# Kernel tuning notes

Measured on AMD Instinct MI355X. Metric: run time of the kernel, lower is better.

## Reference

```python
import jax, jax.numpy as jnp
import numpy as np

V, D, H, L, F, S, HI, DI, TOPK = 50257, 1024, 16, 8, 4096, 1024, 4, 64, 512
DH = D // H
EPS = 1e-6


def rmsnorm(x, w):
    # matches torch: norm = ||x||_2 * D^-0.5 ; out = w * x / (norm + eps)
    n = jnp.linalg.norm(x, axis=-1, keepdims=True) * (x.shape[-1] ** -0.5)
    return w * (x / (n + EPS))


def setup_inputs() -> dict:
    key = jax.random.key(0)
    ks = jax.random.split(key, 16)
    std = 0.02
    tokens = jax.random.randint(ks[0], (2, S), 0, V)
    embed_w = jax.random.normal(ks[1], (V, D), jnp.float32) * std
    pos_w = jax.random.normal(ks[2], (S, D), jnp.float32) * std
    wq = jax.random.normal(ks[3], (L, D, D), jnp.float32) * std
    wk = jax.random.normal(ks[4], (L, D, D), jnp.float32) * std
    wv = jax.random.normal(ks[5], (L, D, D), jnp.float32) * std
    wo = jax.random.normal(ks[6], (L, D, D), jnp.float32) * std
    iq = jax.random.normal(ks[7], (L, D, HI * DI), jnp.float32) * std
    ik = jax.random.normal(ks[8], (L, D, DI), jnp.float32) * std
    iw = jax.random.normal(ks[9], (L, D, HI), jnp.float32) * std
    w1 = jax.random.normal(ks[10], (L, D, F), jnp.float32) * std
    w2 = jax.random.normal(ks[11], (L, F, D), jnp.float32) * std
    norm1 = jnp.ones((L, D), jnp.float32)
    norm2 = jnp.ones((L, D), jnp.float32)
    norm_f = jnp.ones((D,), jnp.float32)
    return dict(tokens=tokens, embed_w=embed_w, pos_w=pos_w, wq=wq, wk=wk,
                wv=wv, wo=wo, iq=iq, ik=ik, iw=iw, w1=w1, w2=w2,
                norm1=norm1, norm2=norm2, norm_f=norm_f)


def _block(x, p, causal):
    (wq, wk, wv, wo, iq, ik, iw, w1, w2, n1, n2) = p
    B = x.shape[0]
    NEG = jnp.finfo(x.dtype).min
    h = rmsnorm(x, n1)
    # --- lightning indexer: scores [B, S, S] ---
    qi = (h @ iq).reshape(B, S, HI, DI)          # [B,S,HI,DI]
    ki = h @ ik                                   # [B,S,DI]
    wt = h @ iw                                   # [B,S,HI]
    idx_logits = jax.nn.relu(jnp.einsum('bqhd,bkd->bhqk', qi, ki))
    idx_scores = jnp.einsum('bqh,bhqk->bqk', wt, idx_logits)  # [B,S,S]
    masked_idx = jnp.where(causal, idx_scores, NEG)
    _, top_i = jax.lax.top_k(masked_idx, TOPK)    # [B,S,TOPK]
    bi = jnp.arange(B)[:, None, None]
    qix = jnp.arange(S)[None, :, None]
    topk_mask = jnp.zeros((B, S, S), bool).at[bi, qix, top_i].set(True)
    allowed = causal & topk_mask                  # [B,S,S]
    # --- sparse multi-head attention (masked dense form, same math) ---
    q = (h @ wq).reshape(B, S, H, DH)
    k = (h @ wk).reshape(B, S, H, DH)
    v = (h @ wv).reshape(B, S, H, DH)
    att = jnp.einsum('bqhd,bkhd->bhqk', q, k) / jnp.sqrt(jnp.float32(DH))
    att = jnp.where(allowed[:, None, :, :], att, NEG)
    p_att = jax.nn.softmax(att, axis=-1)
    out = jnp.einsum('bhqk,bkhd->bqhd', p_att, v).reshape(B, S, D) @ wo
    x = x + out
    # --- feed-forward (exact GELU as nn.GELU) ---
    h2 = rmsnorm(x, n2)
    x = x + jax.nn.gelu(h2 @ w1, approximate=False) @ w2
    return x


def reference(tokens, embed_w, pos_w, wq, wk, wv, wo, iq, ik, iw, w1, w2,
              norm1, norm2, norm_f):
    x = embed_w[tokens] + pos_w[None, :tokens.shape[1], :]
    causal = jnp.tril(jnp.ones((S, S), bool))[None]  # [1,S,S]

    def step(x, p):
        return _block(x, p, causal), None

    x, _ = jax.lax.scan(step, x, (wq, wk, wv, wo, iq, ik, iw, w1, w2, norm1, norm2))
    x = rmsnorm(x, norm_f)
    logits = x @ embed_w.T  # tied lm_head
    return logits
```

## Files before the change

kernel.cpp:

```cpp
#include <hip/hip_runtime.h>
#include <cstdint>
#include <cstddef>

#define S_LEN 1024
#define D_DIM 1024
#define NH 16
#define DHD 64
#define NL 8
#define FF_DIM 4096
#define HI_N 4
#define DI_N 64
#define TOPK_N 512
#define BSROWS 2048
#define VOCAB 50257
#define VPAD 50304
#define NTILES_V 393
#define YPX 50

#define QKV_LD 3072
#define IDX_LD 384
#define COL_QI 0
#define COL_KI 256
#define COL_WT 320

#define NEGF -3.0e38f

typedef __attribute__((ext_vector_type(8))) _Float16 half8;
typedef __attribute__((ext_vector_type(4))) _Float16 half4v;
typedef __attribute__((ext_vector_type(4))) float f32x4;

#if __has_builtin(__builtin_amdgcn_mfma_f32_16x16x16f16)
#define MFMA16F(a, b, c) __builtin_amdgcn_mfma_f32_16x16x16f16((a), (b), (c), 0, 0, 0)
#else
static __device__ __forceinline__ f32x4 mfma16f_asm(half4v a, half4v b, f32x4 c) {
  f32x4 d;
  asm volatile("v_mfma_f32_16x16x16_f16 %0, %1, %2, %3\n\ts_nop 7\n\ts_nop 7"
               : "=v"(d) : "v"(a), "v"(b), "v"(c));
  return d;
}
#define MFMA16F(a, b, c) mfma16f_asm((a), (b), (c))
#endif

typedef const __attribute__((address_space(1))) void* gas_ptr;
typedef __attribute__((address_space(3))) void* las_ptr;
__device__ __forceinline__ void gload16(const void* g, void* l) {
#if __has_builtin(__builtin_amdgcn_global_load_lds)
  __builtin_amdgcn_global_load_lds((gas_ptr)g, (las_ptr)l, 16, 0, 0);
#else
  *(uint4*)l = *(const uint4*)g;
#endif
}

__device__ __forceinline__ short f2h(float x) {
  _Float16 h = (_Float16)x;
  return *reinterpret_cast<short*>(&h);
}
__device__ __forceinline__ float h2f(short b) {
  _Float16 h = *reinterpret_cast<_Float16*>(&b);
  return (float)h;
}
__device__ __forceinline__ void split_h(float x, short& hi, short& lo) {
  hi = f2h(x);
  lo = f2h(x - h2f(hi));
}

__global__ __launch_bounds__(256) void embed_kernel(
    const int* __restrict__ tokens, const float* __restrict__ E,
    const float* __restrict__ P, float* __restrict__ X)
{
  int bs = blockIdx.x;
  int s = bs & (S_LEN - 1);
  int tid = threadIdx.x;
  int tok = tokens[bs];
  float4 e = ((const float4*)(E + (size_t)tok * D_DIM))[tid];
  float4 p = ((const float4*)(P + (size_t)s * D_DIM))[tid];
  float4 o; o.x = e.x + p.x; o.y = e.y + p.y; o.z = e.z + p.z; o.w = e.w + p.w;
  ((float4*)(X + (size_t)bs * D_DIM))[tid] = o;
}

__global__ __launch_bounds__(256) void cvt_embed_kernel(
    const float* __restrict__ E, short* __restrict__ Eh)
{
  const long valid4 = (long)VOCAB * D_DIM / 4;
  const long total4 = (long)VPAD * D_DIM / 4;
  long i = (long)blockIdx.x * 256 + threadIdx.x;
  long stride = (long)gridDim.x * 256;
  for (; i < total4; i += stride) {
    short4 o = make_short4(0, 0, 0, 0);
    if (i < valid4) {
      float4 v = ((const float4*)E)[i];
      o = make_short4(f2h(v.x), f2h(v.y), f2h(v.z), f2h(v.w));
    }
    ((short4*)Eh)[i] = o;
  }
}

__global__ __launch_bounds__(256) void rmsnorm_split_kernel(
    const float* __restrict__ X, const float* __restrict__ W,
    short* __restrict__ O )
{
  int r = blockIdx.x;
  int tid = threadIdx.x;
  float4 v = ((const float4*)(X + (size_t)r * D_DIM))[tid];
  float ss = v.x * v.x + v.y * v.y + v.z * v.z + v.w * v.w;
  __shared__ float red[4];
  __shared__ float sh_inv;
  for (int o = 32; o; o >>= 1) ss += __shfl_down(ss, o);
  if ((tid & 63) == 0) red[tid >> 6] = ss;
  __syncthreads();
  if (tid == 0) {
    float s = red[0] + red[1] + red[2] + red[3];
    sh_inv = 1.0f / (sqrtf(s) * 0.03125f + 1e-6f);
  }
  __syncthreads();
  float inv = sh_inv;
  float4 w = ((const float4*)W)[tid];
  float o0 = w.x * v.x * inv, o1 = w.y * v.y * inv;
  float o2 = w.z * v.z * inv, o3 = w.w * v.w * inv;
  short4 hi, lo;
  split_h(o0, hi.x, lo.x); split_h(o1, hi.y, lo.y);
  split_h(o2, hi.z, lo.z); split_h(o3, hi.w, lo.w);
  ((short4*)(O + (size_t)r * D_DIM))[tid] = hi;
  ((short4*)(O + (size_t)BSROWS * D_DIM + (size_t)r * D_DIM))[tid] = lo;
}

__global__ __launch_bounds__(256) void rmsnorm_h_kernel(
    const float* __restrict__ X, const float* __restrict__ W, short* __restrict__ O)
{
  int r = blockIdx.x;
  int tid = threadIdx.x;
  float4 v = ((const float4*)(X + (size_t)r * D_DIM))[tid];
  float ss = v.x * v.x + v.y * v.y + v.z * v.z + v.w * v.w;
  __shared__ float red[4];
  __shared__ float sh_inv;
  for (int o = 32; o; o >>= 1) ss += __shfl_down(ss, o);
  if ((tid & 63) == 0) red[tid >> 6] = ss;
  __syncthreads();
  if (tid == 0) {
    float s = red[0] + red[1] + red[2] + red[3];
    sh_inv = 1.0f / (sqrtf(s) * 0.03125f + 1e-6f);
  }
  __syncthreads();
  float inv = sh_inv;
  float4 w = ((const float4*)W)[tid];
  short4 o4 = make_short4(f2h(w.x * v.x * inv), f2h(w.y * v.y * inv),
                          f2h(w.z * v.z * inv), f2h(w.w * v.w * inv));
  ((short4*)(O + (size_t)r * D_DIM))[tid] = o4;
}

__global__ __launch_bounds__(256) void packT_all_kernel(
    const float* __restrict__ W0, short* __restrict__ BT0, int K, int N)
{
  __shared__ float t[32][33];
  int z = blockIdx.z;
  const float* W = W0 + (size_t)z * K * N;
  short* BT = BT0 + (size_t)z * N * K;
  int n0 = blockIdx.x * 32, k0 = blockIdx.y * 32;
  int tx = threadIdx.x, ty = threadIdx.y;
#pragma unroll
  for (int r = 0; r < 32; r += 8)
    t[ty + r][tx] = W[(size_t)(k0 + ty + r) * N + n0 + tx];
  __syncthreads();
#pragma unroll
  for (int r = 0; r < 32; r += 8)
    BT[(size_t)(n0 + ty + r) * K + k0 + tx] = f2h(t[tx][ty + r]);
}

__global__ __launch_bounds__(256) void pack_qkv_all_kernel(
    const float* __restrict__ wq0, const float* __restrict__ wk0,
    const float* __restrict__ wv0, short* __restrict__ BT0)
{
  __shared__ float t[32][33];
  int z = blockIdx.z;
  const float* wq = wq0 + (size_t)z * D_DIM * D_DIM;
  const float* wk = wk0 + (size_t)z * D_DIM * D_DIM;
  const float* wv = wv0 + (size_t)z * D_DIM * D_DIM;
  short* BT = BT0 + (size_t)z * QKV_LD * D_DIM;
  int n0 = blockIdx.x * 32, k0 = blockIdx.y * 32;
  int tx = threadIdx.x, ty = threadIdx.y;
  const float* src = (n0 < 1024) ? wq : (n0 < 2048) ? wk : wv;
  int c0 = n0 & 1023;
#pragma unroll
  for (int r = 0; r < 32; r += 8)
    t[ty + r][tx] = src[(size_t)(k0 + ty + r) * 1024 + c0 + tx];
  __syncthreads();
#pragma unroll
  for (int r = 0; r < 32; r += 8)
    BT[(size_t)(n0 + ty + r) * D_DIM + k0 + tx] = f2h(t[tx][ty + r]);
}

__global__ __launch_bounds__(256) void pack_idx_all_kernel(
    const float* __restrict__ iq0, const float* __restrict__ ik0,
    const float* __restrict__ iw0, short* __restrict__ BT0)
{
  __shared__ float t[32][33];
  const size_t plane = (size_t)IDX_LD * D_DIM;
  int z = blockIdx.z;
  const float* iq = iq0 + (size_t)z * D_DIM * (HI_N * DI_N);
  const float* ik = ik0 + (size_t)z * D_DIM * DI_N;
  const float* iw = iw0 + (size_t)z * D_DIM * HI_N;
  short* BT = BT0 + (size_t)z * 2 * plane;
  int n0 = blockIdx.x * 32, k0 = blockIdx.y * 32;
  int tx = threadIdx.x, ty = threadIdx.y;
  const float* src = nullptr; int ld = 0, c0 = 0;
  if (n0 < 256)      { src = iq; ld = 256; c0 = n0; }
  else if (n0 < 320) { src = ik; ld = 64;  c0 = n0 - 256; }
  else if (n0 < 352) { src = iw; ld = 4;   c0 = n0 - 320; }
#pragma unroll
  for (int r = 0; r < 32; r += 8) {
    float v = 0.f;
    int c = c0 + tx;
    if (src && c < ld) v = src[(size_t)(k0 + ty + r) * ld + c];
    t[ty + r][tx] = v;
  }
  __syncthreads();
#pragma unroll
  for (int r = 0; r < 32; r += 8) {
    short hi, lo;
    split_h(t[tx][ty + r], hi, lo);
    size_t o = (size_t)(n0 + ty + r) * D_DIM + k0 + tx;
    BT[o] = hi;
    BT[plane + o] = lo;
  }
}

#define RA 40

template<int BM>
__global__ __launch_bounds__(256) void gemm_split_kernel(
    const short* __restrict__ A, size_t aplane,
    const short* __restrict__ BT, size_t bplane,
    float* __restrict__ C, int M, int N, int K)
{
  constexpr int MI = BM / 32;
  __shared__ short Al[2 * BM * RA];
  __shared__ short Bl[2 * 128 * RA];
  int tid = threadIdx.x;
  int wave = tid >> 6, lane = tid & 63;
  int wr = (wave >> 1) * (BM / 2), wc = (wave & 1) * 64;
  int lr = lane & 15, lk = lane >> 4;
  int m0 = blockIdx.y * BM, n0 = blockIdx.x * 128;
  f32x4 acc[MI][4] = {};

  for (int k0 = 0; k0 < K; k0 += 32) {
    __syncthreads();
#pragma unroll
    for (int f = 0; f < BM / 32; ++f) {
      int idx = tid + f * 256;
      int p = idx / (BM * 4), r2 = idx % (BM * 4);
      int row = r2 >> 2, sub = r2 & 3;
      uint4 v = *(const uint4*)(A + (size_t)p * aplane + (size_t)(m0 + row) * K + k0 + sub * 8);
      *(uint4*)(Al + p * BM * RA + row * RA + sub * 8) = v;
    }
#pragma unroll
    for (int f = 0; f < 4; ++f) {
      int idx = tid + f * 256;
      int p = idx >> 9, r2 = idx & 511;
      int row = r2 >> 2, sub = r2 & 3;
      uint4 v = *(const uint4*)(BT + (size_t)p * bplane + (size_t)(n0 + row) * K + k0 + sub * 8);
      *(uint4*)(Bl + p * 128 * RA + row * RA + sub * 8) = v;
    }
    __syncthreads();
    half8 ah[MI], al_[MI], bh[4], bl_[4];
#pragma unroll
    for (int i = 0; i < MI; ++i) {
      ah[i] = *(const half8*)(Al + (wr + i * 16 + lr) * RA + lk * 8);
      al_[i] = *(const half8*)(Al + BM * RA + (wr + i * 16 + lr) * RA + lk * 8);
    }
#pragma unroll
    for (int j = 0; j < 4; ++j) {
      bh[j] = *(const half8*)(Bl + (wc + j * 16 + lr) * RA + lk * 8);
      bl_[j] = *(const half8*)(Bl + 128 * RA + (wc + j * 16 + lr) * RA + lk * 8);
    }
#pragma unroll
    for (int i = 0; i < MI; ++i)
#pragma unroll
      for (int j = 0; j < 4; ++j) {
        f32x4 a = acc[i][j];
        a = __builtin_amdgcn_mfma_f32_16x16x32_f16(al_[i], bh[j], a, 0, 0, 0);
        a = __builtin_amdgcn_mfma_f32_16x16x32_f16(ah[i], bl_[j], a, 0, 0, 0);
        a = __builtin_amdgcn_mfma_f32_16x16x32_f16(ah[i], bh[j], a, 0, 0, 0);
        acc[i][j] = a;
      }
  }
#pragma unroll
  for (int i = 0; i < MI; ++i)
#pragma unroll
    for (int r = 0; r < 4; ++r) {
      int m = m0 + wr + i * 16 + lk * 4 + r;
#pragma unroll
      for (int j = 0; j < 4; ++j) {
        int n = n0 + wc + j * 16 + lr;
        if (n < N) C[(size_t)m * N + n] = acc[i][j][r];
      }
    }
}

template<int BM, int EPI>
__global__ __launch_bounds__(256) void gemm_g_kernel(
    const short* __restrict__ A, const short* __restrict__ BT,
    const float* __restrict__ R, void* __restrict__ C, int M, int N, int K)
{
  constexpr int MI = BM / 32;
  constexpr int AF = (BM >= 64) ? BM / 64 : 1;
  __shared__ short Al[BM * 32];
  __shared__ short Bl[128 * 32];
  int tid = threadIdx.x;
  int wave = tid >> 6, lane = tid & 63;
  int wr = (wave >> 1) * (BM / 2), wc = (wave & 1) * 64;
  int lr = lane & 15, lk = lane >> 4;
  int m0 = blockIdx.y * BM, n0 = blockIdx.x * 128;
  f32x4 acc[MI][4] = {};

  const short* ap[AF]; short* ad[AF];
#pragma unroll
  for (int f = 0; f < AF; ++f) {
    int idx = tid + f * 256;
    int row = idx >> 2, slot = idx & 3;
    ap[f] = A + (size_t)(m0 + row) * K + ((slot ^ (row & 3)) * 8);
    ad[f] = Al + idx * 8;
  }
  const bool a_act = (BM >= 64) || (tid < BM * 4);
  const short* bp[2]; short* bd[2];
#pragma unroll
  for (int f = 0; f < 2; ++f) {
    int idx = tid + f * 256;
    int row = idx >> 2, slot = idx & 3;
    bp[f] = BT + (size_t)(n0 + row) * K + ((slot ^ (row & 3)) * 8);
    bd[f] = Bl + idx * 8;
  }
  int aoff[MI], boff[4];
#pragma unroll
  for (int i = 0; i < MI; ++i) {
    int row = wr + i * 16 + lr;
    aoff[i] = row * 32 + ((lk ^ (row & 3)) * 8);
  }
#pragma unroll
  for (int j = 0; j < 4; ++j) {
    int row = wc + j * 16 + lr;
    boff[j] = row * 32 + ((lk ^ (row & 3)) * 8);
  }

  for (int k0 = 0; k0 < K; k0 += 32) {
    __syncthreads();
#pragma unroll
    for (int f = 0; f < AF; ++f)
      if (a_act) { gload16(ap[f], ad[f]); ap[f] += 32; }
#pragma unroll
    for (int f = 0; f < 2; ++f) { gload16(bp[f], bd[f]); bp[f] += 32; }
    __syncthreads();
    half8 af[MI], bfr[4];
#pragma unroll
    for (int i = 0; i < MI; ++i) af[i] = *(const half8*)(Al + aoff[i]);
#pragma unroll
    for (int j = 0; j < 4; ++j) bfr[j] = *(const half8*)(Bl + boff[j]);
#pragma unroll
    for (int i = 0; i < MI; ++i)
#pragma unroll
      for (int j = 0; j < 4; ++j)
        acc[i][j] = __builtin_amdgcn_mfma_f32_16x16x32_f16(af[i], bfr[j], acc[i][j], 0, 0, 0);
  }
#pragma unroll
  for (int i = 0; i < MI; ++i)
#pragma unroll
    for (int r = 0; r < 4; ++r) {
      int m = m0 + wr + i * 16 + lk * 4 + r;
#pragma unroll
      for (int j = 0; j < 4; ++j) {
        int n = n0 + wc + j * 16 + lr;
        float v = acc[i][j][r];
        if (EPI == 1) {
          ((short*)C)[(size_t)m * N + n] = f2h(v);
        } else if (EPI == 2) {
          v = 0.5f * v * (1.0f + erff(v * 0.70710678118654752f));
          ((short*)C)[(size_t)m * N + n] = f2h(v);
        } else {
          ((float*)C)[(size_t)m * N + n] = v + R[(size_t)m * N + n];
        }
      }
    }
}

__global__ __launch_bounds__(256) void gemm_logits_g_kernel(
    const short* __restrict__ A, const short* __restrict__ BT,
    float* __restrict__ C, int M, int N, int K)
{
  int bid = blockIdx.x;
  int xcd = bid & 7, idx0 = bid >> 3;
  int mt = idx0 & 15, yt = (idx0 >> 4) + xcd * YPX;
  if (yt >= NTILES_V) return;
  int m0 = mt * 128, n0 = yt * 128;

  __shared__ short Al[128 * 32];
  __shared__ short Bl[128 * 32];
  int tid = threadIdx.x;
  int wave = tid >> 6, lane = tid & 63;
  int wr = (wave >> 1) * 64, wc = (wave & 1) * 64;
  int lr = lane & 15, lk = lane >> 4;
  f32x4 acc[4][4] = {};

  const short* ap[2]; short* ad[2];
  const short* bp[2]; short* bd[2];
#pragma unroll
  for (int f = 0; f < 2; ++f) {
    int idx = tid + f * 256;
    int row = idx >> 2, slot = idx & 3;
    ap[f] = A + (size_t)(m0 + row) * K + ((slot ^ (row & 3)) * 8);
    ad[f] = Al + idx * 8;
    bp[f] = BT + (size_t)(n0 + row) * K + ((slot ^ (row & 3)) * 8);
    bd[f] = Bl + idx * 8;
  }
  int aoff[4], boff[4];
#pragma unroll
  for (int i = 0; i < 4; ++i) {
    int row = wr + i * 16 + lr;
    aoff[i] = row * 32 + ((lk ^ (row & 3)) * 8);
    int rowb = wc + i * 16 + lr;
    boff[i] = rowb * 32 + ((lk ^ (rowb & 3)) * 8);
  }

  for (int k0 = 0; k0 < K; k0 += 32) {
    __syncthreads();
#pragma unroll
    for (int f = 0; f < 2; ++f) { gload16(ap[f], ad[f]); ap[f] += 32; }
#pragma unroll
    for (int f = 0; f < 2; ++f) { gload16(bp[f], bd[f]); bp[f] += 32; }
    __syncthreads();
    half8 af[4], bfr[4];
#pragma unroll
    for (int i = 0; i < 4; ++i) af[i] = *(const half8*)(Al + aoff[i]);
#pragma unroll
    for (int j = 0; j < 4; ++j) bfr[j] = *(const half8*)(Bl + boff[j]);
#pragma unroll
    for (int i = 0; i < 4; ++i)
#pragma unroll
      for (int j = 0; j < 4; ++j)
        acc[i][j] = __builtin_amdgcn_mfma_f32_16x16x32_f16(af[i], bfr[j], acc[i][j], 0, 0, 0);
  }
#pragma unroll
  for (int i = 0; i < 4; ++i)
#pragma unroll
    for (int r = 0; r < 4; ++r) {
      int m = m0 + wr + i * 16 + lk * 4 + r;
#pragma unroll
      for (int j = 0; j < 4; ++j) {
        int n = n0 + wc + j * 16 + lr;
        if (n < N) C[(size_t)m * N + n] = acc[i][j][r];
      }
    }
}

__global__ __launch_bounds__(256) void gemm_logits_f32b_kernel(
    const short* __restrict__ A, const float* __restrict__ BT,
    float* __restrict__ C, int M, int N, int K)
{
  __shared__ short Al[128 * RA];
  __shared__ short Bl[128 * RA];
  int tid = threadIdx.x;
  int wave = tid >> 6, lane = tid & 63;
  int wr = (wave >> 1) * 64, wc = (wave & 1) * 64;
  int lr = lane & 15, lk = lane >> 4;
  int m0 = blockIdx.y * 128, n0 = blockIdx.x * 128;
  f32x4 acc[4][4] = {};

  for (int k0 = 0; k0 < K; k0 += 32) {
    __syncthreads();
#pragma unroll
    for (int f = 0; f < 2; ++f) {
      int idx = tid + f * 256, row = idx >> 2, sub = idx & 3;
      uint4 v = *(const uint4*)(A + (size_t)(m0 + row) * K + k0 + sub * 8);
      *(uint4*)(Al + row * RA + sub * 8) = v;
    }
#pragma unroll
    for (int f = 0; f < 4; ++f) {
      int idx = tid + f * 256, row = idx >> 3, qq = idx & 7;
      int gn = n0 + row;
      float4 v = make_float4(0.f, 0.f, 0.f, 0.f);
      if (gn < N) v = *(const float4*)(BT + (size_t)gn * K + k0 + qq * 4);
      *(short4*)(Bl + row * RA + qq * 4) =
          make_short4(f2h(v.x), f2h(v.y), f2h(v.z), f2h(v.w));
    }
    __syncthreads();
    half8 af[4], bfr[4];
#pragma unroll
    for (int i = 0; i < 4; ++i)
      af[i] = *(const half8*)(Al + (wr + i * 16 + lr) * RA + lk * 8);
#pragma unroll
    for (int j = 0; j < 4; ++j)
      bfr[j] = *(const half8*)(Bl + (wc + j * 16 + lr) * RA + lk * 8);
#pragma unroll
    for (int i = 0; i < 4; ++i)
#pragma unroll
      for (int j = 0; j < 4; ++j)
        acc[i][j] = __builtin_amdgcn_mfma_f32_16x16x32_f16(af[i], bfr[j], acc[i][j], 0, 0, 0);
  }
#pragma unroll
  for (int i = 0; i < 4; ++i)
#pragma unroll
    for (int r = 0; r < 4; ++r) {
      int m = m0 + wr + i * 16 + lk * 4 + r;
#pragma unroll
      for (int j = 0; j < 4; ++j) {
        int n = n0 + wc + j * 16 + lr;
        if (n < N) C[(size_t)m * N + n] = acc[i][j][r];
      }
    }
}

__device__ __forceinline__ unsigned int ford(float f) {
  unsigned int u = __float_as_uint(f);
  return (u & 0x80000000u) ? ~u : (u | 0x80000000u);
}

__global__ __launch_bounds__(256) void idx_topk_kernel(
    const float* __restrict__ Hx, unsigned int* __restrict__ MASK)
{
  int bq = blockIdx.x;
  int q = bq & (S_LEN - 1);
  int b = bq >> 10;
  int tid = threadIdx.x;
  int n = q + 1;
  if (n <= TOPK_N) {
    if (tid < 32) {
      int full = n >> 5, rem = n & 31;
      unsigned int w = 0u;
      if (tid < full) w = 0xFFFFFFFFu;
      else if (tid == full && rem) w = (1u << rem) - 1u;
      MASK[(size_t)bq * 32 + tid] = w;
    }
    return;
  }
  __shared__ float qi_s[HI_N * DI_N];
  __shared__ float wt_s[HI_N];
  __shared__ float sc[S_LEN];
  __shared__ unsigned long long keys[S_LEN];
  __shared__ unsigned int mw[32];
  qi_s[tid] = Hx[(size_t)bq * IDX_LD + COL_QI + tid];
  if (tid < HI_N) wt_s[tid] = Hx[(size_t)bq * IDX_LD + COL_WT + tid];
  __syncthreads();
  for (int k = tid; k < n; k += 256) {
    const float* kr = Hx + (size_t)(b * S_LEN + k) * IDX_LD + COL_KI;
    float d0 = 0.f, d1 = 0.f, d2 = 0.f, d3 = 0.f;
#pragma unroll
    for (int d = 0; d < DI_N; ++d) {
      float kv = kr[d];
      d0 = fmaf(qi_s[d], kv, d0);
      d1 = fmaf(qi_s[64 + d], kv, d1);
      d2 = fmaf(qi_s[128 + d], kv, d2);
      d3 = fmaf(qi_s[192 + d], kv, d3);
    }
    sc[k] = wt_s[0] * fmaxf(d0, 0.f) + wt_s[1] * fmaxf(d1, 0.f)
          + wt_s[2] * fmaxf(d2, 0.f) + wt_s[3] * fmaxf(d3, 0.f);
  }
  __syncthreads();
  for (int i = tid; i < S_LEN; i += 256) {
    unsigned long long kk = 0ull;
    if (i < n) kk = ((unsigned long long)ford(sc[i]) << 32) | (unsigned int)(S_LEN - 1 - i);
    keys[i] = kk;
  }
  __syncthreads();
  for (int size = 2; size <= S_LEN; size <<= 1) {
    for (int stride = size >> 1; stride > 0; stride >>= 1) {
      for (int t = tid; t < S_LEN / 2; t += 256) {
        int j = t & (stride - 1);
        int lo = ((t ^ j) << 1) | j;
        int hi = lo | stride;
        unsigned long long a = keys[lo], c = keys[hi];
        bool desc = ((lo & size) == 0);
        bool sw = desc ? (a < c) : (a > c);
        if (sw) { keys[lo] = c; keys[hi] = a; }
      }
      __syncthreads();
    }
  }
  if (tid < 32) mw[tid] = 0u;
  __syncthreads();
  for (int i = tid; i < TOPK_N; i += 256) {
    int k = S_LEN - 1 - (int)(keys[i] & 0xFFFFFFFFull);
    atomicOr(&mw[k >> 5], 1u << (k & 31));
  }
  __syncthreads();
  if (tid < 32) MASK[(size_t)bq * 32 + tid] = mw[tid];
}

__global__ __launch_bounds__(256) void attn_mfma_kernel(
    const short* __restrict__ QKV, const unsigned int* __restrict__ MASK,
    short* __restrict__ O )
{
  __shared__ unsigned int mlds[64 * 32];
  __shared__ short Kl[2][64 * 64];
  __shared__ short Vtl[2][64 * 68];
  int i = blockIdx.x;
  int p = i >> 5;
  int qt = (p < 8) ? p : 23 - p;
  int h = (i >> 1) & 15;
  int b = i & 1;
  int tid = threadIdx.x;
  int w = tid >> 6, l = tid & 63;
  int lq = l & 15, g = l >> 4;
  int q0 = qt * 64;
  const short* Kb = QKV + (size_t)b * S_LEN * QKV_LD + 1024 + h * DHD;
  const short* Vb = QKV + (size_t)b * S_LEN * QKV_LD + 2048 + h * DHD;
  int vu = tid >> 1, vhalf = tid & 1, vkg = vu >> 3, vdg = vu & 7;

#pragma unroll
  for (int i2 = 0; i2 < 8; ++i2) {
    int idx = tid + i2 * 256;
    mlds[idx] = MASK[((size_t)(b * S_LEN + q0 + (idx >> 5))) * 32 + (idx & 31)];
  }
  half8 qf[2];
  {
    const short* qrow = QKV + ((size_t)(b * S_LEN + q0 + w * 16 + lq)) * QKV_LD + h * DHD;
    qf[0] = *(const half8*)(qrow + g * 8);
    qf[1] = *(const half8*)(qrow + 32 + g * 8);
  }
  {
#pragma unroll
    for (int i2 = 0; i2 < 2; ++i2) {
      int idx = tid + i2 * 256;
      int row = idx >> 3, sub = idx & 7;
      gload16(Kb + (size_t)row * QKV_LD + (size_t)((sub ^ (row & 7)) * 8), &Kl[0][idx * 8]);
    }
    int krow = vkg * 4 + vhalf * 2;
    uint4 v0 = *(const uint4*)(Vb + (size_t)krow * QKV_LD + vdg * 8);
    uint4 v1 = *(const uint4*)(Vb + (size_t)(krow + 1) * QKV_LD + vdg * 8);
    const short* s0 = (const short*)&v0;
    const short* s1 = (const short*)&v1;
#pragma unroll
    for (int j = 0; j < 8; ++j)
      *(short2*)(&Vtl[0][(vdg * 8 + j) * 68 + vkg * 4 + vhalf * 2]) = make_short2(s0[j], s1[j]);
  }
  __syncthreads();

  f32x4 acc_o[4] = {};
  float m_run = -1.0e30f, l_run = 0.f;
  const int mrow = w * 16 + lq;
  int cur = 0;

  for (int kt = 0; kt <= qt; ++kt) {
    bool more = kt < qt;
    uint4 v0, v1;
    if (more) {
#pragma unroll
      for (int i2 = 0; i2 < 2; ++i2) {
        int idx = tid + i2 * 256;
        int row = idx >> 3, sub = idx & 7;
        gload16(Kb + (size_t)((kt + 1) * 64 + row) * QKV_LD + (size_t)((sub ^ (row & 7)) * 8),
                &Kl[cur ^ 1][idx * 8]);
      }
      int krow = (kt + 1) * 64 + vkg * 4 + vhalf * 2;
      v0 = *(const uint4*)(Vb + (size_t)krow * QKV_LD + vdg * 8);
      v1 = *(const uint4*)(Vb + (size_t)(krow + 1) * QKV_LD + vdg * 8);
    }
    f32x4 s[4] = {};
    __builtin_amdgcn_s_setprio(1);
#pragma unroll
    for (int ks = 0; ks < 4; ++ks) {
      half8 kf0 = *(const half8*)(&Kl[cur][(ks * 16 + lq) * 64 + ((g ^ (lq & 7)) * 8)]);
      half8 kf1 = *(const half8*)(&Kl[cur][(ks * 16 + lq) * 64 + (((4 + g) ^ (lq & 7)) * 8)]);
      s[ks] = __builtin_amdgcn_mfma_f32_16x16x32_f16(kf0, qf[0], s[ks], 0, 0, 0);
      s[ks] = __builtin_amdgcn_mfma_f32_16x16x32_f16(kf1, qf[1], s[ks], 0, 0, 0);
    }
    __builtin_amdgcn_s_setprio(0);
    float mx = NEGF;
#pragma unroll
    for (int ks = 0; ks < 4; ++ks) {
      int kbase = kt * 64 + ks * 16 + g * 4;
      unsigned mwv = mlds[mrow * 32 + (kbase >> 5)];
#pragma unroll
      for (int r = 0; r < 4; ++r) {
        float sv = ((mwv >> ((kbase + r) & 31)) & 1u) ? s[ks][r] * 0.125f : NEGF;
        s[ks][r] = sv;
        mx = fmaxf(mx, sv);
      }
    }
    mx = fmaxf(mx, __shfl_xor(mx, 16));
    mx = fmaxf(mx, __shfl_xor(mx, 32));
    float m_new = fmaxf(m_run, mx);
    float scale = __expf(m_run - m_new);
    float lsum = 0.f;
    half4v pf[4];
#pragma unroll
    for (int ks = 0; ks < 4; ++ks) {
      half4v t;
#pragma unroll
      for (int r = 0; r < 4; ++r) {
        float pp = __expf(s[ks][r] - m_new);
        lsum += pp;
        t[r] = (_Float16)pp;
      }
      pf[ks] = t;
    }
    lsum += __shfl_xor(lsum, 16);
    lsum += __shfl_xor(lsum, 32);
    l_run = l_run * scale + lsum;
    m_run = m_new;
    float sc[4];
#pragma unroll
    for (int r = 0; r < 4; ++r) sc[r] = __shfl(scale, g * 4 + r);
    __builtin_amdgcn_s_setprio(1);
#pragma unroll
    for (int dt = 0; dt < 4; ++dt) {
      f32x4 a = acc_o[dt];
      a[0] *= sc[0]; a[1] *= sc[1]; a[2] *= sc[2]; a[3] *= sc[3];
#pragma unroll
      for (int ks = 0; ks < 4; ++ks) {
        half4v vf = *(const half4v*)(&Vtl[cur][(dt * 16 + lq) * 68 + ks * 16 + g * 4]);
        a = MFMA16F(pf[ks], vf, a);
      }
      acc_o[dt] = a;
    }
    __builtin_amdgcn_s_setprio(0);
    if (more) {
      const short* s0 = (const short*)&v0;
      const short* s1 = (const short*)&v1;
#pragma unroll
      for (int j = 0; j < 8; ++j)
        *(short2*)(&Vtl[cur ^ 1][(vdg * 8 + j) * 68 + vkg * 4 + vhalf * 2]) = make_short2(s0[j], s1[j]);
    }
    __syncthreads();
    cur ^= 1;
  }
  float linv[4];
#pragma unroll
  for (int r = 0; r < 4; ++r) linv[r] = 1.0f / __shfl(l_run, g * 4 + r);
#pragma unroll
  for (int dt = 0; dt < 4; ++dt)
#pragma unroll
    for (int r = 0; r < 4; ++r) {
      int q = q0 + w * 16 + g * 4 + r;
      float o = acc_o[dt][r] * linv[r];
      O[(size_t)(b * S_LEN + q) * D_DIM + h * DHD + dt * 16 + lq] = f2h(o);
    }
}

extern "C" void kernel_launch(void* const* d_in, const int* in_sizes, int n_in,
                              void* d_out, int out_size, void* d_ws, size_t ws_size,
                              hipStream_t stream) {
  (void)in_sizes; (void)n_in; (void)out_size;
  const int*   tokens  = (const int*)d_in[0];
  const float* embed_w = (const float*)d_in[1];
  const float* pos_w   = (const float*)d_in[2];
  const float* wq      = (const float*)d_in[3];
  const float* wk      = (const float*)d_in[4];
  const float* wv      = (const float*)d_in[5];
  const float* wo      = (const float*)d_in[6];
  const float* iqw     = (const float*)d_in[7];
  const float* ikw     = (const float*)d_in[8];
  const float* iww     = (const float*)d_in[9];
  const float* w1      = (const float*)d_in[10];
  const float* w2      = (const float*)d_in[11];
  const float* n1      = (const float*)d_in[12];
  const float* n2      = (const float*)d_in[13];
  const float* nf      = (const float*)d_in[14];
  float* logits = (float*)d_out;

  short* Hh = (short*)d_ws;
  size_t need_eh = ((size_t)BSROWS * D_DIM + (size_t)VPAD * D_DIM) * 2;
  bool use_eh = ws_size >= need_eh;
  short* Eh = Hh + (size_t)BSROWS * D_DIM;

  char* base = (char*)d_out;
  size_t off = (size_t)BSROWS * D_DIM * 4;
  float* X = logits;
  float* Hx = (float*)(base + off);    off += (size_t)BSROWS * IDX_LD * 4;
  short* QKVh = (short*)(base + off);  off += (size_t)BSROWS * QKV_LD * 2;
  short* Hsp = (short*)(base + off);   off += (size_t)2 * BSROWS * D_DIM * 2;
  short* AOh = (short*)(base + off);   off += (size_t)BSROWS * D_DIM * 2;
  short* FFh = (short*)(base + off);   off += (size_t)BSROWS * FF_DIM * 2;
  unsigned int* MASKb = (unsigned int*)(base + off); off += (size_t)BSROWS * 32 * 4;
  short* BTqkvA = (short*)(base + off); off += (size_t)NL * QKV_LD * D_DIM * 2;
  short* BTidxA = (short*)(base + off); off += (size_t)NL * 2 * IDX_LD * D_DIM * 2;
  short* BTwoA = (short*)(base + off);  off += (size_t)NL * D_DIM * D_DIM * 2;
  short* BTw1A = (short*)(base + off);  off += (size_t)NL * FF_DIM * D_DIM * 2;
  short* BTw2A = (short*)(base + off);  off += (size_t)NL * FF_DIM * D_DIM * 2;

  const size_t plH  = (size_t)BSROWS * D_DIM;
  const size_t plIx = (size_t)IDX_LD * D_DIM;

  hipLaunchKernelGGL(embed_kernel, dim3(BSROWS), dim3(256), 0, stream,
                     tokens, embed_w, pos_w, X);
  if (use_eh)
    hipLaunchKernelGGL(cvt_embed_kernel, dim3(8192), dim3(256), 0, stream, embed_w, Eh);

  hipLaunchKernelGGL(pack_qkv_all_kernel, dim3(QKV_LD / 32, 32, NL), dim3(32, 8), 0, stream,
                     wq, wk, wv, BTqkvA);
  hipLaunchKernelGGL(pack_idx_all_kernel, dim3(IDX_LD / 32, 32, NL), dim3(32, 8), 0, stream,
                     iqw, ikw, iww, BTidxA);
  hipLaunchKernelGGL(packT_all_kernel, dim3(32, 32, NL), dim3(32, 8), 0, stream,
                     wo, BTwoA, D_DIM, D_DIM);
  hipLaunchKernelGGL(packT_all_kernel, dim3(FF_DIM / 32, 32, NL), dim3(32, 8), 0, stream,
                     w1, BTw1A, D_DIM, FF_DIM);
  hipLaunchKernelGGL(packT_all_kernel, dim3(D_DIM / 32, FF_DIM / 32, NL), dim3(32, 8), 0, stream,
                     w2, BTw2A, FF_DIM, D_DIM);

  for (int l = 0; l < NL; ++l) {
    short* BTqkv = BTqkvA + (size_t)l * QKV_LD * D_DIM;
    short* BTidx = BTidxA + (size_t)l * 2 * IDX_LD * D_DIM;
    short* BTwo  = BTwoA + (size_t)l * D_DIM * D_DIM;
    short* BTw1  = BTw1A + (size_t)l * FF_DIM * D_DIM;
    short* BTw2  = BTw2A + (size_t)l * FF_DIM * D_DIM;

    hipLaunchKernelGGL(rmsnorm_split_kernel, dim3(BSROWS), dim3(256), 0, stream,
                       X, n1 + (size_t)l * D_DIM, Hsp);
    hipLaunchKernelGGL((gemm_g_kernel<64, 1>), dim3(QKV_LD / 128, 32), dim3(256), 0, stream,
                       Hsp, BTqkv, nullptr, QKVh, BSROWS, QKV_LD, D_DIM);
    hipLaunchKernelGGL((gemm_split_kernel<32>), dim3(IDX_LD / 128, 64), dim3(256), 0, stream,
                       Hsp, plH, BTidx, plIx, Hx, BSROWS, IDX_LD, D_DIM);
    hipLaunchKernelGGL(idx_topk_kernel, dim3(BSROWS), dim3(256), 0, stream, Hx, MASKb);
    hipLaunchKernelGGL(attn_mfma_kernel, dim3(512), dim3(256), 0, stream,
                       QKVh, MASKb, AOh);
    hipLaunchKernelGGL((gemm_g_kernel<32, 3>), dim3(8, 64), dim3(256), 0, stream,
                       AOh, BTwo, X, X, BSROWS, D_DIM, D_DIM);
    hipLaunchKernelGGL(rmsnorm_h_kernel, dim3(BSROWS), dim3(256), 0, stream,
                       X, n2 + (size_t)l * D_DIM, Hsp);
    hipLaunchKernelGGL((gemm_g_kernel<64, 2>), dim3(FF_DIM / 128, 32), dim3(256), 0, stream,
                       Hsp, BTw1, nullptr, FFh, BSROWS, FF_DIM, D_DIM);
    hipLaunchKernelGGL((gemm_g_kernel<32, 3>), dim3(8, 64), dim3(256), 0, stream,
                       FFh, BTw2, X, X, BSROWS, D_DIM, FF_DIM);
  }

  hipLaunchKernelGGL(rmsnorm_h_kernel, dim3(BSROWS), dim3(256), 0, stream, X, nf, Hh);
  if (use_eh) {
    hipLaunchKernelGGL(gemm_logits_g_kernel, dim3(8 * YPX * 16), dim3(256), 0, stream,
                       Hh, Eh, logits, BSROWS, VOCAB, D_DIM);
  } else {
    hipLaunchKernelGGL(gemm_logits_f32b_kernel, dim3((VOCAB + 127) / 128, 16), dim3(256), 0, stream,
                       Hh, embed_w, logits, BSROWS, VOCAB, D_DIM);
  }
}
```

Measured before the change: 3.419 ms.

## Double-buffer GEMM LDS tiles and stream attention mask words through registers

After: 3.299 ms (median of 2 runs). 1.04x faster.

```diff
diff --git a/kernel.cpp b/kernel.cpp
--- a/kernel.cpp
+++ b/kernel.cpp
@@ -303,8 +303,8 @@
 {
   constexpr int MI = BM / 32;
   constexpr int AF = (BM >= 64) ? BM / 64 : 1;
-  __shared__ short Al[BM * 32];
-  __shared__ short Bl[128 * 32];
+  __shared__ short Al[2][BM * 32];
+  __shared__ short Bl[2][128 * 32];
   int tid = threadIdx.x;
   int wave = tid >> 6, lane = tid & 63;
   int wr = (wave >> 1) * (BM / 2), wc = (wave & 1) * 64;
@@ -312,22 +312,22 @@
   int m0 = blockIdx.y * BM, n0 = blockIdx.x * 128;
   f32x4 acc[MI][4] = {};
 
-  const short* ap[AF]; short* ad[AF];
+  const short* ap[AF]; int ad[AF];
 #pragma unroll
   for (int f = 0; f < AF; ++f) {
     int idx = tid + f * 256;
     int row = idx >> 2, slot = idx & 3;
     ap[f] = A + (size_t)(m0 + row) * K + ((slot ^ (row & 3)) * 8);
-    ad[f] = Al + idx * 8;
+    ad[f] = idx * 8;
   }
   const bool a_act = (BM >= 64) || (tid < BM * 4);
-  const short* bp[2]; short* bd[2];
+  const short* bp[2]; int bd[2];
 #pragma unroll
   for (int f = 0; f < 2; ++f) {
     int idx = tid + f * 256;
     int row = idx >> 2, slot = idx & 3;
     bp[f] = BT + (size_t)(n0 + row) * K + ((slot ^ (row & 3)) * 8);
-    bd[f] = Bl + idx * 8;
+    bd[f] = idx * 8;
   }
   int aoff[MI], boff[4];
 #pragma unroll
@@ -341,24 +341,35 @@
     boff[j] = row * 32 + ((lk ^ (row & 3)) * 8);
   }
 
-  for (int k0 = 0; k0 < K; k0 += 32) {
-    __syncthreads();
-#pragma unroll
-    for (int f = 0; f < AF; ++f)
-      if (a_act) { gload16(ap[f], ad[f]); ap[f] += 32; }
-#pragma unroll
-    for (int f = 0; f < 2; ++f) { gload16(bp[f], bd[f]); bp[f] += 32; }
-    __syncthreads();
+#pragma unroll
+  for (int f = 0; f < AF; ++f)
+    if (a_act) { gload16(ap[f], &Al[0][ad[f]]); ap[f] += 32; }
+#pragma unroll
+  for (int f = 0; f < 2; ++f) { gload16(bp[f], &Bl[0][bd[f]]); bp[f] += 32; }
+  __syncthreads();
+
+  const int nt = K >> 5;
+  int cur = 0;
+  for (int t = 0; t < nt; ++t) {
+    if (t + 1 < nt) {
+#pragma unroll
+      for (int f = 0; f < AF; ++f)
+        if (a_act) { gload16(ap[f], &Al[cur ^ 1][ad[f]]); ap[f] += 32; }
+#pragma unroll
+      for (int f = 0; f < 2; ++f) { gload16(bp[f], &Bl[cur ^ 1][bd[f]]); bp[f] += 32; }
+    }
     half8 af[MI], bfr[4];
 #pragma unroll
-    for (int i = 0; i < MI; ++i) af[i] = *(const half8*)(Al + aoff[i]);
-#pragma unroll
-    for (int j = 0; j < 4; ++j) bfr[j] = *(const half8*)(Bl + boff[j]);
+    for (int i = 0; i < MI; ++i) af[i] = *(const half8*)(&Al[cur][aoff[i]]);
+#pragma unroll
+    for (int j = 0; j < 4; ++j) bfr[j] = *(const half8*)(&Bl[cur][boff[j]]);
 #pragma unroll
     for (int i = 0; i < MI; ++i)
 #pragma unroll
       for (int j = 0; j < 4; ++j)
         acc[i][j] = __builtin_amdgcn_mfma_f32_16x16x32_f16(af[i], bfr[j], acc[i][j], 0, 0, 0);
+    __syncthreads();
+    cur ^= 1;
   }
 #pragma unroll
   for (int i = 0; i < MI; ++i)
@@ -391,24 +402,24 @@
   if (yt >= NTILES_V) return;
   int m0 = mt * 128, n0 = yt * 128;
 
-  __shared__ short Al[128 * 32];
-  __shared__ short Bl[128 * 32];
+  __shared__ short Al[2][128 * 32];
+  __shared__ short Bl[2][128 * 32];
   int tid = threadIdx.x;
   int wave = tid >> 6, lane = tid & 63;
   int wr = (wave >> 1) * 64, wc = (wave & 1) * 64;
   int lr = lane & 15, lk = lane >> 4;
   f32x4 acc[4][4] = {};
 
-  const short* ap[2]; short* ad[2];
-  const short* bp[2]; short* bd[2];
+  const short* ap[2]; int ad[2];
+  const short* bp[2]; int bd[2];
 #pragma unroll
   for (int f = 0; f < 2; ++f) {
     int idx = tid + f * 256;
     int row = idx >> 2, slot = idx & 3;
     ap[f] = A + (size_t)(m0 + row) * K + ((slot ^ (row & 3)) * 8);
-    ad[f] = Al + idx * 8;
+    ad[f] = idx * 8;
     bp[f] = BT + (size_t)(n0 + row) * K + ((slot ^ (row & 3)) * 8);
-    bd[f] = Bl + idx * 8;
+    bd[f] = idx * 8;
   }
   int aoff[4], boff[4];
 #pragma unroll
@@ -419,23 +430,33 @@
     boff[i] = rowb * 32 + ((lk ^ (rowb & 3)) * 8);
   }
 
-  for (int k0 = 0; k0 < K; k0 += 32) {
-    __syncthreads();
-#pragma unroll
-    for (int f = 0; f < 2; ++f) { gload16(ap[f], ad[f]); ap[f] += 32; }
-#pragma unroll
-    for (int f = 0; f < 2; ++f) { gload16(bp[f], bd[f]); bp[f] += 32; }
-    __syncthreads();
+#pragma unroll
+  for (int f = 0; f < 2; ++f) { gload16(ap[f], &Al[0][ad[f]]); ap[f] += 32; }
+#pragma unroll
+  for (int f = 0; f < 2; ++f) { gload16(bp[f], &Bl[0][bd[f]]); bp[f] += 32; }
+  __syncthreads();
+
+  const int nt = K >> 5;
+  int cur = 0;
+  for (int t = 0; t < nt; ++t) {
+    if (t + 1 < nt) {
+#pragma unroll
+      for (int f = 0; f < 2; ++f) { gload16(ap[f], &Al[cur ^ 1][ad[f]]); ap[f] += 32; }
+#pragma unroll
+      for (int f = 0; f < 2; ++f) { gload16(bp[f], &Bl[cur ^ 1][bd[f]]); bp[f] += 32; }
+    }
     half8 af[4], bfr[4];
 #pragma unroll
-    for (int i = 0; i < 4; ++i) af[i] = *(const half8*)(Al + aoff[i]);
-#pragma unroll
-    for (int j = 0; j < 4; ++j) bfr[j] = *(const half8*)(Bl + boff[j]);
+    for (int i = 0; i < 4; ++i) af[i] = *(const half8*)(&Al[cur][aoff[i]]);
+#pragma unroll
+    for (int j = 0; j < 4; ++j) bfr[j] = *(const half8*)(&Bl[cur][boff[j]]);
 #pragma unroll
     for (int i = 0; i < 4; ++i)
 #pragma unroll
       for (int j = 0; j < 4; ++j)
         acc[i][j] = __builtin_amdgcn_mfma_f32_16x16x32_f16(af[i], bfr[j], acc[i][j], 0, 0, 0);
+    __syncthreads();
+    cur ^= 1;
   }
 #pragma unroll
   for (int i = 0; i < 4; ++i)
@@ -587,7 +608,6 @@
     const short* __restrict__ QKV, const unsigned int* __restrict__ MASK,
     short* __restrict__ O )
 {
-  __shared__ unsigned int mlds[64 * 32];
   __shared__ short Kl[2][64 * 64];
   __shared__ short Vtl[2][64 * 68];
   int i = blockIdx.x;
@@ -602,18 +622,16 @@
   const short* Kb = QKV + (size_t)b * S_LEN * QKV_LD + 1024 + h * DHD;
   const short* Vb = QKV + (size_t)b * S_LEN * QKV_LD + 2048 + h * DHD;
   int vu = tid >> 1, vhalf = tid & 1, vkg = vu >> 3, vdg = vu & 7;
-
-#pragma unroll
-  for (int i2 = 0; i2 < 8; ++i2) {
-    int idx = tid + i2 * 256;
-    mlds[idx] = MASK[((size_t)(b * S_LEN + q0 + (idx >> 5))) * 32 + (idx & 31)];
-  }
+  const int mrow = w * 16 + lq;
+  const unsigned int* mp = MASK + (size_t)(b * S_LEN + q0 + mrow) * 32;
+
   half8 qf[2];
   {
-    const short* qrow = QKV + ((size_t)(b * S_LEN + q0 + w * 16 + lq)) * QKV_LD + h * DHD;
+    const short* qrow = QKV + ((size_t)(b * S_LEN + q0 + mrow)) * QKV_LD + h * DHD;
     qf[0] = *(const half8*)(qrow + g * 8);
     qf[1] = *(const half8*)(qrow + 32 + g * 8);
   }
+  unsigned int mw0 = mp[0], mw1 = mp[1];
   {
 #pragma unroll
     for (int i2 = 0; i2 < 2; ++i2) {
@@ -634,12 +652,12 @@
 
   f32x4 acc_o[4] = {};
   float m_run = -1.0e30f, l_run = 0.f;
-  const int mrow = w * 16 + lq;
   int cur = 0;
 
   for (int kt = 0; kt <= qt; ++kt) {
     bool more = kt < qt;
     uint4 v0, v1;
+    unsigned int nmw0 = 0u, nmw1 = 0u;
     if (more) {
 #pragma unroll
       for (int i2 = 0; i2 < 2; ++i2) {
@@ -651,6 +669,8 @@
       int krow = (kt + 1) * 64 + vkg * 4 + vhalf * 2;
       v0 = *(const uint4*)(Vb + (size_t)krow * QKV_LD + vdg * 8);
       v1 = *(const uint4*)(Vb + (size_t)(krow + 1) * QKV_LD + vdg * 8);
+      nmw0 = mp[2 * (kt + 1)];
+      nmw1 = mp[2 * (kt + 1) + 1];
     }
     f32x4 s[4] = {};
     __builtin_amdgcn_s_setprio(1);
@@ -665,11 +685,11 @@
     float mx = NEGF;
 #pragma unroll
     for (int ks = 0; ks < 4; ++ks) {
-      int kbase = kt * 64 + ks * 16 + g * 4;
-      unsigned mwv = mlds[mrow * 32 + (kbase >> 5)];
+      unsigned int mwv = (ks < 2) ? mw0 : mw1;
+      int bb = (ks & 1) * 16 + g * 4;
 #pragma unroll
       for (int r = 0; r < 4; ++r) {
-        float sv = ((mwv >> ((kbase + r) & 31)) & 1u) ? s[ks][r] * 0.125f : NEGF;
+        float sv = ((mwv >> (bb + r)) & 1u) ? s[ks][r] * 0.125f : NEGF;
         s[ks][r] = sv;
         mx = fmaxf(mx, sv);
       }
@@ -717,6 +737,8 @@
 #pragma unroll
       for (int j = 0; j < 8; ++j)
         *(short2*)(&Vtl[cur ^ 1][(vdg * 8 + j) * 68 + vkg * 4 + vhalf * 2]) = make_short2(s0[j], s1[j]);
+      mw0 = nmw0;
+      mw1 = nmw1;
     }
     __syncthreads();
     cur ^= 1;
```
